# Optimization experiments

Hardware: AMD Instinct MI355X
Metric: run time of the kernel (lower is better)

Reference implementation:

```python
import jax, jax.numpy as jnp
import numpy as np

P_X, P_H, P_L, P_VT, P_ET, B = 512, 1024, 4, 512, 256, 512
IN_DIM = P_X + 2 * P_H  # concat([x, prev_time_h, prev_layer_h])


def setup_inputs() -> dict:
    key = jax.random.key(0)
    ks = jax.random.split(key, 10)
    sc_in = 1.0 / np.sqrt(IN_DIM)
    sc_lh = 1.0 / np.sqrt(P_L * P_H)
    return {
        "input_x": jax.random.normal(ks[0], (B, P_X), jnp.float32),
        "h_prev": jax.random.normal(ks[1], (P_L, B, P_H), jnp.float32),
        "c_prev": jax.random.normal(ks[2], (P_L, B, P_H), jnp.float32),
        # stacked gate weights: [L, 4 gates (i,f,o,s), h, in_dim]
        "Wg": jax.random.uniform(ks[3], (P_L, 4, P_H, IN_DIM), jnp.float32, -sc_in, sc_in),
        "bg": jax.random.uniform(ks[4], (P_L, 4, P_H), jnp.float32, -sc_in, sc_in),
        "W_y": jax.random.uniform(ks[5], (P_VT, P_L * P_H), jnp.float32, -sc_lh, sc_lh),
        "b_y": jax.random.uniform(ks[6], (P_VT,), jnp.float32, -sc_lh, sc_lh),
        "W_E": jax.random.uniform(ks[7], (P_ET, P_L * P_H), jnp.float32, -sc_lh, sc_lh),
        "b_E": jax.random.uniform(ks[8], (P_ET,), jnp.float32, -sc_lh, sc_lh),
    }


def _controller(input_x, h_prev, c_prev, Wg, bg):
    prev_layer = jnp.zeros((input_x.shape[0], P_H), input_x.dtype)
    hiddens = []
    for i in range(P_L):  # loop over small fixed layer count
        z = jnp.concatenate([input_x, h_prev[i], prev_layer], axis=-1)  # [B, IN_DIM]
        g = jnp.einsum("bd,ghd->bgh", z, Wg[i]) + bg[i]  # [B, 4, H], one fused GEMM
        i_g = jax.nn.sigmoid(g[:, 0])
        f_g = jax.nn.sigmoid(g[:, 1])
        o_g = jax.nn.sigmoid(g[:, 2])
        s_g = jnp.tanh(g[:, 3])
        c_new = f_g * c_prev[i] + i_g * s_g
        h_new = o_g * jnp.tanh(c_new)
        hiddens.append(h_new)
        prev_layer = h_new
    return jnp.concatenate(hiddens, axis=-1)  # [B, L*H]


def reference(input_x, h_prev, c_prev, Wg, bg, W_y, b_y, W_E, b_E):
    hidden = _controller(input_x, h_prev, c_prev, Wg, bg)
    output = hidden @ W_y.T + b_y      # [B, v_t]
    interface = hidden @ W_E.T + b_E   # [B, E_t]
    return (output, interface)
```

## Files before the change

kernel.cpp:

```cpp
#include <hip/hip_runtime.h>


typedef short    shortx8  __attribute__((ext_vector_type(8)));
typedef float    floatx4  __attribute__((ext_vector_type(4)));
typedef float    floatx16 __attribute__((ext_vector_type(16)));

__device__ __forceinline__ unsigned int f2bf1(float x) {
  unsigned int u = __float_as_uint(x);
  return (u + 0x7fffu + ((u >> 16) & 1u)) >> 16;
}
__device__ __forceinline__ unsigned int f2bf2(float lo, float hi) {
  return f2bf1(lo) | (f2bf1(hi) << 16);
}
__device__ __forceinline__ float sigm(float x) { return 1.f / (1.f + __expf(-x)); }
__device__ __forceinline__ float tanh_(float x) { return 1.f - 2.f / (__expf(2.f * x) + 1.f); }

__global__ __launch_bounds__(256) void prep_a0(const float* __restrict__ x,
                                               const float* __restrict__ hp,
                                               unsigned short* __restrict__ A0) {
  const int l   = blockIdx.y;
  const int idx = blockIdx.x * 256 + threadIdx.x;
  const int b   = idx / 192;
  const int kk  = (idx - b * 192) * 8;
  float v[8];
  if (kk < 512) {
    const float* s = x + (size_t)b * 512 + kk;
#pragma unroll
    for (int i = 0; i < 8; ++i) v[i] = s[i];
  } else {
    const float* s = hp + ((size_t)l * 512 + b) * 1024 + (kk - 512);
#pragma unroll
    for (int i = 0; i < 8; ++i) v[i] = s[i];
  }
  uint4 o;
  o.x = f2bf2(v[0], v[1]); o.y = f2bf2(v[2], v[3]);
  o.z = f2bf2(v[4], v[5]); o.w = f2bf2(v[6], v[7]);
  *(uint4*)(A0 + ((size_t)l * 512 + b) * 1536 + kk) = o;
}

__global__ __launch_bounds__(256) void conv_wseq(const float* __restrict__ Wg,
                                                 unsigned short* __restrict__ Wseq) {
  const int idx = blockIdx.x * 256 + threadIdx.x;
  const int row = idx >> 7;
  const int k0  = (idx & 127) * 8;
  const int l   = (row >> 12) + 1;
  const int n   = row & 4095;
  const float* s = Wg + (size_t)l * 4096 * 2560 + (size_t)n * 2560 + 1536 + k0;
  const float4 v0 = *(const float4*)(s);
  const float4 v1 = *(const float4*)(s + 4);
  uint4 o;
  o.x = f2bf2(v0.x, v0.y); o.y = f2bf2(v0.z, v0.w);
  o.z = f2bf2(v1.x, v1.y); o.w = f2bf2(v1.z, v1.w);
  *(uint4*)(Wseq + (size_t)row * 1024 + k0) = o;
}

__global__ __launch_bounds__(256, 2) void gemm_gates(
    const unsigned short* __restrict__ A0, const float* __restrict__ Wg,
    const float* __restrict__ bg, float* __restrict__ G) {
  __shared__ __align__(16) unsigned short As[2][128 * 64];
  __shared__ __align__(16) unsigned short Bs[2][128 * 64];
  const int tid = threadIdx.x, lane = tid & 63, wave = tid >> 6;
  const int raw   = blockIdx.x + 4 * (blockIdx.y + 32 * blockIdx.z);
  const int xcd   = raw & 7, slot = raw >> 3;
  const int nl    = (slot >> 2) * 8 + xcd;
  const int mbase = (slot & 3) * 128;
  const int nbase = (nl & 31) * 128;
  const int l     = nl >> 5;
  const unsigned short* Ab = A0 + ((size_t)l * 512 + mbase) * 1536;
  const float*          Bb = Wg + (size_t)l * 4096 * 2560 + (size_t)nbase * 2560;
  const int arow = wave * 8 + (lane >> 3);
  const int akg  = lane & 7;

  uint4  apf[4];
  float4 bpf[8];
  auto loadT = [&](int kt) {
    const int kg = kt * 64;
#pragma unroll
    for (int r = 0; r < 4; ++r)
      apf[r] = *(const uint4*)(Ab + (size_t)(arow + r * 32) * 1536 + kg + akg * 8);
#pragma unroll
    for (int j = 0; j < 8; ++j) {
      const int idx = j * 256 + tid;
      bpf[j] = *(const float4*)(Bb + (size_t)(idx >> 4) * 2560 + kg + (idx & 15) * 4);
    }
  };
  auto storeT = [&](int buf) {
#pragma unroll
    for (int r = 0; r < 4; ++r) {
      const int row = arow + r * 32;
      *(uint4*)(&As[buf][row * 64 + ((akg ^ (row & 7)) * 8)]) = apf[r];
    }
#pragma unroll
    for (int j = 0; j < 8; ++j) {
      const int idx = j * 256 + tid;
      const int n = idx >> 4, kc = (idx & 15) * 4;
      uint2 pk;
      pk.x = f2bf2(bpf[j].x, bpf[j].y);
      pk.y = f2bf2(bpf[j].z, bpf[j].w);
      *(uint2*)(&Bs[buf][n * 64 + (((kc >> 3) ^ (n & 7)) * 8) + (kc & 4)]) = pk;
    }
  };

  floatx16 acc[2][2];
#pragma unroll
  for (int a = 0; a < 2; ++a)
#pragma unroll
    for (int b2 = 0; b2 < 2; ++b2)
#pragma unroll
      for (int r = 0; r < 16; ++r) acc[a][b2][r] = 0.f;

  const int wm = (wave >> 1) * 64, wn = (wave & 1) * 64;
  loadT(0);
  storeT(0);
  __syncthreads();
  for (int kt = 0; kt < 24; ++kt) {
    if (kt + 1 < 24) loadT(kt + 1);
    const int cb = kt & 1;
#pragma unroll
    for (int ks = 0; ks < 4; ++ks) {
      const int gb = ks * 2 + (lane >> 5);
      shortx8 af[2], bfv[2];
#pragma unroll
      for (int sm = 0; sm < 2; ++sm) {
        const int row = wm + sm * 32 + (lane & 31);
        af[sm] = *(const shortx8*)(&As[cb][row * 64 + ((gb ^ (row & 7)) * 8)]);
      }
#pragma unroll
      for (int sn = 0; sn < 2; ++sn) {
        const int row = wn + sn * 32 + (lane & 31);
        bfv[sn] = *(const shortx8*)(&Bs[cb][row * 64 + ((gb ^ (row & 7)) * 8)]);
      }
#pragma unroll
      for (int sm = 0; sm < 2; ++sm)
#pragma unroll
        for (int sn = 0; sn < 2; ++sn)
          acc[sm][sn] = __builtin_amdgcn_mfma_f32_32x32x16_bf16(
              af[sm], bfv[sn], acc[sm][sn], 0, 0, 0);
    }
    if (kt + 1 < 24) storeT((kt + 1) & 1);
    __syncthreads();
  }

  const float* bgl = bg + (size_t)l * 4096;
  float* Gl = G + ((size_t)l * 512 + mbase) * 4096;
#pragma unroll
  for (int sm = 0; sm < 2; ++sm)
#pragma unroll
    for (int sn = 0; sn < 2; ++sn) {
      const int col = nbase + wn + sn * 32 + (lane & 31);
      const float bias = bgl[col];
#pragma unroll
      for (int r = 0; r < 16; ++r) {
        const int row = wm + sm * 32 + ((r & 3) + 8 * (r >> 2) + 4 * (lane >> 5));
        Gl[(size_t)row * 4096 + col] = acc[sm][sn][r] + bias;
      }
    }
}

__global__ __launch_bounds__(256) void cell0(const float* __restrict__ G,
                                             const float* __restrict__ cp_l,
                                             unsigned short* __restrict__ hidden) {
  const int idx = (blockIdx.x * 256 + threadIdx.x) * 4;
  const int b = idx >> 10, h = idx & 1023;
  const float* g0 = G + (size_t)b * 4096;
  const float4 vi = *(const float4*)(g0 + h);
  const float4 vf = *(const float4*)(g0 + 1024 + h);
  const float4 vo = *(const float4*)(g0 + 2048 + h);
  const float4 vs = *(const float4*)(g0 + 3072 + h);
  const float4 cp = *(const float4*)(cp_l + (size_t)b * 1024 + h);
  const float gi[4] = {vi.x, vi.y, vi.z, vi.w};
  const float gf[4] = {vf.x, vf.y, vf.z, vf.w};
  const float go[4] = {vo.x, vo.y, vo.z, vo.w};
  const float gs[4] = {vs.x, vs.y, vs.z, vs.w};
  const float cc[4] = {cp.x, cp.y, cp.z, cp.w};
  float hn[4];
#pragma unroll
  for (int j = 0; j < 4; ++j) {
    const float c = sigm(gf[j]) * cc[j] + sigm(gi[j]) * tanh_(gs[j]);
    hn[j] = sigm(go[j]) * tanh_(c);
  }
  uint2 o;
  o.x = f2bf2(hn[0], hn[1]);
  o.y = f2bf2(hn[2], hn[3]);
  *(uint2*)(hidden + (size_t)b * 4096 + h) = o;
}

__global__ __launch_bounds__(256) void seq_stream(
    const unsigned short* __restrict__ hidden_ro,
    const unsigned short* __restrict__ Wseq,
    const float* __restrict__ G, const float* __restrict__ c_prev,
    unsigned short* __restrict__ hidden_w, int l) {
  const int tid = threadIdx.x, lane = tid & 63, wv = tid >> 6;
  const int bid = blockIdx.x;
  const int x   = bid & 7;
  const int mg  = (bid >> 3) & 7;
  const int t   = bid >> 6;
  const int ht  = x * 8 + t;
  const int mt  = mg * 4 + wv;
  const int mb  = mt * 16, h0 = ht * 16;
  const int lrow = lane & 15, lg = lane >> 4;

  const unsigned short* Ab = hidden_ro + (size_t)(mb + lrow) * 4096
                             + (size_t)(l - 1) * 1024 + lg * 8;
  const unsigned short* Bb = Wseq + (size_t)(l - 1) * 4194304
                             + (size_t)(h0 + lrow) * 1024 + lg * 8;

  const int brow = mb + lg * 4;
  const int hg   = h0 + lrow;
  float gvv[4][4];
  float cold[4];
#pragma unroll
  for (int r = 0; r < 4; ++r) {
    const float* Gb = G + ((size_t)l * 512 + brow + r) * 4096 + hg;
#pragma unroll
    for (int g = 0; g < 4; ++g) gvv[g][r] = Gb[g * 1024];
    cold[r] = c_prev[((size_t)l * 512 + brow + r) * 1024 + hg];
  }

  floatx4 acc0, acc1, acc2, acc3;
#pragma unroll
  for (int r = 0; r < 4; ++r) { acc0[r] = 0.f; acc1[r] = 0.f; acc2[r] = 0.f; acc3[r] = 0.f; }

  shortx8 a0, a1, a2, a3;
  shortx8 b00, b01, b02, b03;
  shortx8 b10, b11, b12, b13;
  shortx8 b20, b21, b22, b23;
  shortx8 b30, b31, b32, b33;

#define LD_SET(ai, b0_, b1_, b2_, b3_, kt)                                   \
  {                                                                          \
    const int ko = (kt) * 32;                                                \
    ai  = *(const shortx8*)(Ab + ko);                                        \
    b0_ = *(const shortx8*)(Bb + ko);                                        \
    b1_ = *(const shortx8*)(Bb + 1048576 + ko);                              \
    b2_ = *(const shortx8*)(Bb + 2097152 + ko);                              \
    b3_ = *(const shortx8*)(Bb + 3145728 + ko);                              \
  }
#define C_SET(ai, b0_, b1_, b2_, b3_)                                        \
  {                                                                          \
    acc0 = __builtin_amdgcn_mfma_f32_16x16x32_bf16(ai, b0_, acc0, 0, 0, 0);  \
    acc1 = __builtin_amdgcn_mfma_f32_16x16x32_bf16(ai, b1_, acc1, 0, 0, 0);  \
    acc2 = __builtin_amdgcn_mfma_f32_16x16x32_bf16(ai, b2_, acc2, 0, 0, 0);  \
    acc3 = __builtin_amdgcn_mfma_f32_16x16x32_bf16(ai, b3_, acc3, 0, 0, 0);  \
  }

  LD_SET(a0, b00, b01, b02, b03, 0)
  LD_SET(a1, b10, b11, b12, b13, 1)
  LD_SET(a2, b20, b21, b22, b23, 2)
  LD_SET(a3, b30, b31, b32, b33, 3)
#pragma unroll 1
  for (int kt4 = 0; kt4 < 8; ++kt4) {
    const int kt = kt4 * 4;
    C_SET(a0, b00, b01, b02, b03)
    if (kt + 4 < 32) LD_SET(a0, b00, b01, b02, b03, kt + 4)
    C_SET(a1, b10, b11, b12, b13)
    if (kt + 5 < 32) LD_SET(a1, b10, b11, b12, b13, kt + 5)
    C_SET(a2, b20, b21, b22, b23)
    if (kt + 6 < 32) LD_SET(a2, b20, b21, b22, b23, kt + 6)
    C_SET(a3, b30, b31, b32, b33)
    if (kt + 7 < 32) LD_SET(a3, b30, b31, b32, b33, kt + 7)
  }
#undef LD_SET
#undef C_SET

#pragma unroll
  for (int r = 0; r < 4; ++r) {
    const float gi = acc0[r] + gvv[0][r];
    const float gf = acc1[r] + gvv[1][r];
    const float go = acc2[r] + gvv[2][r];
    const float gs = acc3[r] + gvv[3][r];
    const float c  = sigm(gf) * cold[r] + sigm(gi) * tanh_(gs);
    const float hn = sigm(go) * tanh_(c);
    hidden_w[(size_t)(brow + r) * 4096 + l * 1024 + hg] = (unsigned short)f2bf1(hn);
  }
}

__global__ __launch_bounds__(256) void gemm_heads(
    const unsigned short* __restrict__ A, const float* __restrict__ Wy,
    const float* __restrict__ WE, float* __restrict__ Cp) {
  __shared__ __align__(16) unsigned short As[2][128 * 64];
  __shared__ __align__(16) unsigned short Bs[2][128 * 64];
  const int tid = threadIdx.x, lane = tid & 63, wave = tid >> 6;
  const int rawb = blockIdx.x + 8 * (blockIdx.y + 6 * blockIdx.z);
  const int xcd  = rawb & 7, slot = rawb >> 3;
  const int pair = (slot >> 2) * 8 + xcd;
  const int mbase  = (slot & 3) * 128;
  const int ksplit = pair & 7;
  const int nt     = pair >> 3;
  const int nbase  = nt * 128;
  const float* Bb = (nt < 4) ? (Wy + (size_t)nbase * 4096)
                             : (WE + (size_t)(nbase - 512) * 4096);
  const int k0 = ksplit * 512;
  const unsigned short* Ab = A + (size_t)mbase * 4096;
  const int arow = wave * 8 + (lane >> 3);
  const int akg  = lane & 7;

  uint4  apf[4];
  float4 bpf[8];
  auto loadT = [&](int kt) {
    const int kg = k0 + kt * 64;
#pragma unroll
    for (int r = 0; r < 4; ++r)
      apf[r] = *(const uint4*)(Ab + (size_t)(arow + r * 32) * 4096 + kg + akg * 8);
#pragma unroll
    for (int j = 0; j < 8; ++j) {
      const int idx = j * 256 + tid;
      bpf[j] = *(const float4*)(Bb + (size_t)(idx >> 4) * 4096 + kg + (idx & 15) * 4);
    }
  };
  auto storeT = [&](int buf) {
#pragma unroll
    for (int r = 0; r < 4; ++r) {
      const int row = arow + r * 32;
      *(uint4*)(&As[buf][row * 64 + ((akg ^ (row & 7)) * 8)]) = apf[r];
    }
#pragma unroll
    for (int j = 0; j < 8; ++j) {
      const int idx = j * 256 + tid;
      const int n = idx >> 4, kc = (idx & 15) * 4;
      uint2 pk;
      pk.x = f2bf2(bpf[j].x, bpf[j].y);
      pk.y = f2bf2(bpf[j].z, bpf[j].w);
      *(uint2*)(&Bs[buf][n * 64 + (((kc >> 3) ^ (n & 7)) * 8) + (kc & 4)]) = pk;
    }
  };

  floatx16 acc[2][2];
#pragma unroll
  for (int a = 0; a < 2; ++a)
#pragma unroll
    for (int b2 = 0; b2 < 2; ++b2)
#pragma unroll
      for (int r = 0; r < 16; ++r) acc[a][b2][r] = 0.f;
  const int wm = (wave >> 1) * 64, wn = (wave & 1) * 64;

  loadT(0);
  storeT(0);
  __syncthreads();
  for (int kt = 0; kt < 8; ++kt) {
    if (kt + 1 < 8) loadT(kt + 1);
    const int cb = kt & 1;
#pragma unroll
    for (int ks = 0; ks < 4; ++ks) {
      const int gb = ks * 2 + (lane >> 5);
      shortx8 af[2], bfv[2];
#pragma unroll
      for (int sm = 0; sm < 2; ++sm) {
        const int row = wm + sm * 32 + (lane & 31);
        af[sm] = *(const shortx8*)(&As[cb][row * 64 + ((gb ^ (row & 7)) * 8)]);
      }
#pragma unroll
      for (int sn = 0; sn < 2; ++sn) {
        const int row = wn + sn * 32 + (lane & 31);
        bfv[sn] = *(const shortx8*)(&Bs[cb][row * 64 + ((gb ^ (row & 7)) * 8)]);
      }
#pragma unroll
      for (int sm = 0; sm < 2; ++sm)
#pragma unroll
        for (int sn = 0; sn < 2; ++sn)
          acc[sm][sn] = __builtin_amdgcn_mfma_f32_32x32x16_bf16(
              af[sm], bfv[sn], acc[sm][sn], 0, 0, 0);
    }
    if (kt + 1 < 8) storeT((kt + 1) & 1);
    __syncthreads();
  }

  float* Co = Cp + (size_t)ksplit * 512 * 768;
#pragma unroll
  for (int sm = 0; sm < 2; ++sm)
#pragma unroll
    for (int sn = 0; sn < 2; ++sn) {
      const int col = nbase + wn + sn * 32 + (lane & 31);
#pragma unroll
      for (int r = 0; r < 16; ++r) {
        const int row = mbase + wm + sm * 32 +
                        ((r & 3) + 8 * (r >> 2) + 4 * (lane >> 5));
        Co[(size_t)row * 768 + col] = acc[sm][sn][r];
      }
    }
}

__global__ __launch_bounds__(256) void head_reduce(
    const float* __restrict__ hp, const float* __restrict__ b_y,
    const float* __restrict__ b_E, float* __restrict__ out) {
  const int n = blockIdx.x * 256 + threadIdx.x;
  const int b = blockIdx.y;
  float s = 0.f;
#pragma unroll
  for (int ks = 0; ks < 8; ++ks)
    s += hp[(size_t)ks * 512 * 768 + (size_t)b * 768 + n];
  if (n < 512)
    out[(size_t)b * 512 + n] = s + b_y[n];
  else
    out[(size_t)512 * 512 + (size_t)b * 256 + (n - 512)] = s + b_E[n - 512];
}

extern "C" void kernel_launch(void* const* d_in, const int* in_sizes, int n_in,
                              void* d_out, int out_size, void* d_ws, size_t ws_size,
                              hipStream_t stream) {
  const float* x      = (const float*)d_in[0];
  const float* h_prev = (const float*)d_in[1];
  const float* c_prev = (const float*)d_in[2];
  const float* Wg     = (const float*)d_in[3];
  const float* bg     = (const float*)d_in[4];
  const float* W_y    = (const float*)d_in[5];
  const float* b_y    = (const float*)d_in[6];
  const float* W_E    = (const float*)d_in[7];
  const float* b_E    = (const float*)d_in[8];

  char* ws = (char*)d_ws;
  unsigned short* A0     = (unsigned short*)(ws + 0);
  float*          G      = (float*)(ws + 6291456);
  unsigned short* hidden = (unsigned short*)(ws + 39845888);
  unsigned short* Wseq   = (unsigned short*)(ws + 44040192);
  float*          hpart  = (float*)(ws + 44040192);

  conv_wseq<<<dim3(6144), 256, 0, stream>>>(Wg, Wseq);
  prep_a0<<<dim3(384, 4), 256, 0, stream>>>(x, h_prev, A0);
  gemm_gates<<<dim3(4, 32, 4), 256, 0, stream>>>(A0, Wg, bg, G);
  cell0<<<512, 256, 0, stream>>>(G, c_prev, hidden);
  for (int l = 1; l < 4; ++l)
    seq_stream<<<dim3(512), 256, 0, stream>>>(hidden, Wseq, G, c_prev,
                                              hidden, l);
  gemm_heads<<<dim3(8, 6, 4), 256, 0, stream>>>(hidden, W_y, W_E, hpart);
  head_reduce<<<dim3(3, 512), 256, 0, stream>>>(hpart, b_y, b_E, (float*)d_out);
}
```

Before: 460.3 us.

## Pre-convert all weights to bf16 and stage GEMM tiles via global_load_lds

A single prep kernel now converts all of Wg, W_y and W_E to bf16, together with the A0 activations, replacing the separate conv_wseq and prep_a0 launches. The gates and heads GEMMs then read bf16 weights and stage tiles straight into LDS with global_load_lds, which drops the register round-trip and the in-loop fp32-to-bf16 conversion. seq_stream reads its recurrent weights from the fully converted Wg buffer. In exchange, the prep pass reads and writes far more data, including the unused prev-layer slice of layer 0, and the LDS XOR swizzle is gone, so fragment reads may hit bank conflicts.

Measured after the change: 478.2 us. +3.9%, slower.

```diff
diff --git a/kernel.cpp b/kernel.cpp
--- a/kernel.cpp
+++ b/kernel.cpp
@@ -5,6 +5,11 @@
 typedef float    floatx4  __attribute__((ext_vector_type(4)));
 typedef float    floatx16 __attribute__((ext_vector_type(16)));
 
+#define GLOAD16(SRC, DST)                                                    \
+  __builtin_amdgcn_global_load_lds(                                          \
+      (const __attribute__((address_space(1))) unsigned int*)(SRC),          \
+      (__attribute__((address_space(3))) unsigned int*)(DST), 16, 0, 0)
+
 __device__ __forceinline__ unsigned int f2bf1(float x) {
   unsigned int u = __float_as_uint(x);
   return (u + 0x7fffu + ((u >> 16) & 1u)) >> 16;
@@ -15,47 +20,51 @@
 __device__ __forceinline__ float sigm(float x) { return 1.f / (1.f + __expf(-x)); }
 __device__ __forceinline__ float tanh_(float x) { return 1.f - 2.f / (__expf(2.f * x) + 1.f); }
 
-__global__ __launch_bounds__(256) void prep_a0(const float* __restrict__ x,
-                                               const float* __restrict__ hp,
-                                               unsigned short* __restrict__ A0) {
-  const int l   = blockIdx.y;
-  const int idx = blockIdx.x * 256 + threadIdx.x;
-  const int b   = idx / 192;
-  const int kk  = (idx - b * 192) * 8;
-  float v[8];
-  if (kk < 512) {
-    const float* s = x + (size_t)b * 512 + kk;
-#pragma unroll
-    for (int i = 0; i < 8; ++i) v[i] = s[i];
+__global__ __launch_bounds__(256) void prep_all(
+    const float* __restrict__ x, const float* __restrict__ hp,
+    const float* __restrict__ Wg, const float* __restrict__ Wy,
+    const float* __restrict__ WE, unsigned short* __restrict__ A0,
+    unsigned short* __restrict__ Wc, unsigned short* __restrict__ Wyc,
+    unsigned short* __restrict__ WEc) {
+  const int bid = blockIdx.x;
+  if (bid < 22016) {
+    const size_t i8 = ((size_t)bid * 256 + threadIdx.x) * 8;
+    const float* s;
+    unsigned short* d;
+    if (i8 < 41943040u) { s = Wg + i8; d = Wc + i8; }
+    else if (i8 < 44040192u) { s = Wy + (i8 - 41943040u); d = Wyc + (i8 - 41943040u); }
+    else { s = WE + (i8 - 44040192u); d = WEc + (i8 - 44040192u); }
+    const float4 v0 = *(const float4*)(s);
+    const float4 v1 = *(const float4*)(s + 4);
+    uint4 o;
+    o.x = f2bf2(v0.x, v0.y); o.y = f2bf2(v0.z, v0.w);
+    o.z = f2bf2(v1.x, v1.y); o.w = f2bf2(v1.z, v1.w);
+    *(uint4*)(d) = o;
   } else {
-    const float* s = hp + ((size_t)l * 512 + b) * 1024 + (kk - 512);
-#pragma unroll
-    for (int i = 0; i < 8; ++i) v[i] = s[i];
-  }
-  uint4 o;
-  o.x = f2bf2(v[0], v[1]); o.y = f2bf2(v[2], v[3]);
-  o.z = f2bf2(v[4], v[5]); o.w = f2bf2(v[6], v[7]);
-  *(uint4*)(A0 + ((size_t)l * 512 + b) * 1536 + kk) = o;
-}
-
-__global__ __launch_bounds__(256) void conv_wseq(const float* __restrict__ Wg,
-                                                 unsigned short* __restrict__ Wseq) {
-  const int idx = blockIdx.x * 256 + threadIdx.x;
-  const int row = idx >> 7;
-  const int k0  = (idx & 127) * 8;
-  const int l   = (row >> 12) + 1;
-  const int n   = row & 4095;
-  const float* s = Wg + (size_t)l * 4096 * 2560 + (size_t)n * 2560 + 1536 + k0;
-  const float4 v0 = *(const float4*)(s);
-  const float4 v1 = *(const float4*)(s + 4);
-  uint4 o;
-  o.x = f2bf2(v0.x, v0.y); o.y = f2bf2(v0.z, v0.w);
-  o.z = f2bf2(v1.x, v1.y); o.w = f2bf2(v1.z, v1.w);
-  *(uint4*)(Wseq + (size_t)row * 1024 + k0) = o;
+    const int j   = (bid - 22016) * 256 + threadIdx.x;
+    const int l   = j / 98304;
+    const int rem = j - l * 98304;
+    const int b   = rem / 192;
+    const int kk  = (rem - b * 192) * 8;
+    float v[8];
+    if (kk < 512) {
+      const float* s = x + (size_t)b * 512 + kk;
+#pragma unroll
+      for (int i = 0; i < 8; ++i) v[i] = s[i];
+    } else {
+      const float* s = hp + ((size_t)l * 512 + b) * 1024 + (kk - 512);
+#pragma unroll
+      for (int i = 0; i < 8; ++i) v[i] = s[i];
+    }
+    uint4 o;
+    o.x = f2bf2(v[0], v[1]); o.y = f2bf2(v[2], v[3]);
+    o.z = f2bf2(v[4], v[5]); o.w = f2bf2(v[6], v[7]);
+    *(uint4*)(A0 + ((size_t)l * 512 + b) * 1536 + kk) = o;
+  }
 }
 
 __global__ __launch_bounds__(256, 2) void gemm_gates(
-    const unsigned short* __restrict__ A0, const float* __restrict__ Wg,
+    const unsigned short* __restrict__ A0, const unsigned short* __restrict__ Wc,
     const float* __restrict__ bg, float* __restrict__ G) {
   __shared__ __align__(16) unsigned short As[2][128 * 64];
   __shared__ __align__(16) unsigned short Bs[2][128 * 64];
@@ -67,39 +76,22 @@
   const int nbase = (nl & 31) * 128;
   const int l     = nl >> 5;
   const unsigned short* Ab = A0 + ((size_t)l * 512 + mbase) * 1536;
-  const float*          Bb = Wg + (size_t)l * 4096 * 2560 + (size_t)nbase * 2560;
-  const int arow = wave * 8 + (lane >> 3);
-  const int akg  = lane & 7;
-
-  uint4  apf[4];
-  float4 bpf[8];
-  auto loadT = [&](int kt) {
+  const unsigned short* Bb = Wc + (size_t)l * 4096 * 2560 + (size_t)nbase * 2560;
+  const int wv8 = wave * 8;
+  const int lr  = lane >> 3;
+  const int lc  = (lane & 7) * 8;
+
+  auto stage = [&](int kt, int buf) {
     const int kg = kt * 64;
 #pragma unroll
     for (int r = 0; r < 4; ++r)
-      apf[r] = *(const uint4*)(Ab + (size_t)(arow + r * 32) * 1536 + kg + akg * 8);
-#pragma unroll
-    for (int j = 0; j < 8; ++j) {
-      const int idx = j * 256 + tid;
-      bpf[j] = *(const float4*)(Bb + (size_t)(idx >> 4) * 2560 + kg + (idx & 15) * 4);
-    }
+      GLOAD16(Ab + (size_t)(wv8 + lr + r * 32) * 1536 + kg + lc,
+              &As[buf][(wv8 + r * 32) * 64]);
+#pragma unroll
+    for (int r = 0; r < 4; ++r)
+      GLOAD16(Bb + (size_t)(wv8 + lr + r * 32) * 2560 + kg + lc,
+              &Bs[buf][(wv8 + r * 32) * 64]);
   };
-  auto storeT = [&](int buf) {
-#pragma unroll
-    for (int r = 0; r < 4; ++r) {
-      const int row = arow + r * 32;
-      *(uint4*)(&As[buf][row * 64 + ((akg ^ (row & 7)) * 8)]) = apf[r];
-    }
-#pragma unroll
-    for (int j = 0; j < 8; ++j) {
-      const int idx = j * 256 + tid;
-      const int n = idx >> 4, kc = (idx & 15) * 4;
-      uint2 pk;
-      pk.x = f2bf2(bpf[j].x, bpf[j].y);
-      pk.y = f2bf2(bpf[j].z, bpf[j].w);
-      *(uint2*)(&Bs[buf][n * 64 + (((kc >> 3) ^ (n & 7)) * 8) + (kc & 4)]) = pk;
-    }
-  };
 
   floatx16 acc[2][2];
 #pragma unroll
@@ -110,26 +102,17 @@
       for (int r = 0; r < 16; ++r) acc[a][b2][r] = 0.f;
 
   const int wm = (wave >> 1) * 64, wn = (wave & 1) * 64;
-  loadT(0);
-  storeT(0);
-  __syncthreads();
-  for (int kt = 0; kt < 24; ++kt) {
-    if (kt + 1 < 24) loadT(kt + 1);
-    const int cb = kt & 1;
+  auto compute = [&](int cb) {
 #pragma unroll
     for (int ks = 0; ks < 4; ++ks) {
       const int gb = ks * 2 + (lane >> 5);
       shortx8 af[2], bfv[2];
 #pragma unroll
-      for (int sm = 0; sm < 2; ++sm) {
-        const int row = wm + sm * 32 + (lane & 31);
-        af[sm] = *(const shortx8*)(&As[cb][row * 64 + ((gb ^ (row & 7)) * 8)]);
-      }
-#pragma unroll
-      for (int sn = 0; sn < 2; ++sn) {
-        const int row = wn + sn * 32 + (lane & 31);
-        bfv[sn] = *(const shortx8*)(&Bs[cb][row * 64 + ((gb ^ (row & 7)) * 8)]);
-      }
+      for (int sm = 0; sm < 2; ++sm)
+        af[sm] = *(const shortx8*)(&As[cb][(wm + sm * 32 + (lane & 31)) * 64 + gb * 8]);
+#pragma unroll
+      for (int sn = 0; sn < 2; ++sn)
+        bfv[sn] = *(const shortx8*)(&Bs[cb][(wn + sn * 32 + (lane & 31)) * 64 + gb * 8]);
 #pragma unroll
       for (int sm = 0; sm < 2; ++sm)
 #pragma unroll
@@ -137,7 +120,14 @@
           acc[sm][sn] = __builtin_amdgcn_mfma_f32_32x32x16_bf16(
               af[sm], bfv[sn], acc[sm][sn], 0, 0, 0);
     }
-    if (kt + 1 < 24) storeT((kt + 1) & 1);
+  };
+
+  stage(0, 0);
+  __syncthreads();
+#pragma unroll 1
+  for (int kt = 0; kt < 24; ++kt) {
+    if (kt + 1 < 24) stage(kt + 1, (kt + 1) & 1);
+    compute(kt & 1);
     __syncthreads();
   }
 
@@ -187,7 +177,7 @@
 
 __global__ __launch_bounds__(256) void seq_stream(
     const unsigned short* __restrict__ hidden_ro,
-    const unsigned short* __restrict__ Wseq,
+    const unsigned short* __restrict__ Wc,
     const float* __restrict__ G, const float* __restrict__ c_prev,
     unsigned short* __restrict__ hidden_w, int l) {
   const int tid = threadIdx.x, lane = tid & 63, wv = tid >> 6;
@@ -202,8 +192,8 @@
 
   const unsigned short* Ab = hidden_ro + (size_t)(mb + lrow) * 4096
                              + (size_t)(l - 1) * 1024 + lg * 8;
-  const unsigned short* Bb = Wseq + (size_t)(l - 1) * 4194304
-                             + (size_t)(h0 + lrow) * 1024 + lg * 8;
+  const unsigned short* Bb = Wc + (size_t)l * 4096 * 2560
+                             + (size_t)(h0 + lrow) * 2560 + 1536 + lg * 8;
 
   const int brow = mb + lg * 4;
   const int hg   = h0 + lrow;
@@ -232,9 +222,9 @@
     const int ko = (kt) * 32;                                                \
     ai  = *(const shortx8*)(Ab + ko);                                        \
     b0_ = *(const shortx8*)(Bb + ko);                                        \
-    b1_ = *(const shortx8*)(Bb + 1048576 + ko);                              \
-    b2_ = *(const shortx8*)(Bb + 2097152 + ko);                              \
-    b3_ = *(const shortx8*)(Bb + 3145728 + ko);                              \
+    b1_ = *(const shortx8*)(Bb + 2621440 + ko);                              \
+    b2_ = *(const shortx8*)(Bb + 5242880 + ko);                              \
+    b3_ = *(const shortx8*)(Bb + 7864320 + ko);                              \
   }
 #define C_SET(ai, b0_, b1_, b2_, b3_)                                        \
   {                                                                          \
@@ -275,9 +265,9 @@
   }
 }
 
-__global__ __launch_bounds__(256) void gemm_heads(
-    const unsigned short* __restrict__ A, const float* __restrict__ Wy,
-    const float* __restrict__ WE, float* __restrict__ Cp) {
+__global__ __launch_bounds__(256, 2) void gemm_heads(
+    const unsigned short* __restrict__ A, const unsigned short* __restrict__ Wyc,
+    const unsigned short* __restrict__ WEc, float* __restrict__ Cp) {
   __shared__ __align__(16) unsigned short As[2][128 * 64];
   __shared__ __align__(16) unsigned short Bs[2][128 * 64];
   const int tid = threadIdx.x, lane = tid & 63, wave = tid >> 6;
@@ -288,41 +278,24 @@
   const int ksplit = pair & 7;
   const int nt     = pair >> 3;
   const int nbase  = nt * 128;
-  const float* Bb = (nt < 4) ? (Wy + (size_t)nbase * 4096)
-                             : (WE + (size_t)(nbase - 512) * 4096);
+  const unsigned short* Bb = (nt < 4) ? (Wyc + (size_t)nbase * 4096)
+                                      : (WEc + (size_t)(nbase - 512) * 4096);
   const int k0 = ksplit * 512;
   const unsigned short* Ab = A + (size_t)mbase * 4096;
-  const int arow = wave * 8 + (lane >> 3);
-  const int akg  = lane & 7;
-
-  uint4  apf[4];
-  float4 bpf[8];
-  auto loadT = [&](int kt) {
+  const int wv8 = wave * 8;
+  const int lr  = lane >> 3;
+  const int lc  = (lane & 7) * 8;
+
+  auto stage = [&](int kt, int buf) {
     const int kg = k0 + kt * 64;
 #pragma unroll
     for (int r = 0; r < 4; ++r)
-      apf[r] = *(const uint4*)(Ab + (size_t)(arow + r * 32) * 4096 + kg + akg * 8);
-#pragma unroll
-    for (int j = 0; j < 8; ++j) {
-      const int idx = j * 256 + tid;
-      bpf[j] = *(const float4*)(Bb + (size_t)(idx >> 4) * 4096 + kg + (idx & 15) * 4);
-    }
-  };
-  auto storeT = [&](int buf) {
-#pragma unroll
-    for (int r = 0; r < 4; ++r) {
-      const int row = arow + r * 32;
-      *(uint4*)(&As[buf][row * 64 + ((akg ^ (row & 7)) * 8)]) = apf[r];
-    }
-#pragma unroll
-    for (int j = 0; j < 8; ++j) {
-      const int idx = j * 256 + tid;
-      const int n = idx >> 4, kc = (idx & 15) * 4;
-      uint2 pk;
-      pk.x = f2bf2(bpf[j].x, bpf[j].y);
-      pk.y = f2bf2(bpf[j].z, bpf[j].w);
-      *(uint2*)(&Bs[buf][n * 64 + (((kc >> 3) ^ (n & 7)) * 8) + (kc & 4)]) = pk;
-    }
+      GLOAD16(Ab + (size_t)(wv8 + lr + r * 32) * 4096 + kg + lc,
+              &As[buf][(wv8 + r * 32) * 64]);
+#pragma unroll
+    for (int r = 0; r < 4; ++r)
+      GLOAD16(Bb + (size_t)(wv8 + lr + r * 32) * 4096 + kg + lc,
+              &Bs[buf][(wv8 + r * 32) * 64]);
   };
 
   floatx16 acc[2][2];
@@ -334,26 +307,17 @@
       for (int r = 0; r < 16; ++r) acc[a][b2][r] = 0.f;
   const int wm = (wave >> 1) * 64, wn = (wave & 1) * 64;
 
-  loadT(0);
-  storeT(0);
-  __syncthreads();
-  for (int kt = 0; kt < 8; ++kt) {
-    if (kt + 1 < 8) loadT(kt + 1);
-    const int cb = kt & 1;
+  auto compute = [&](int cb) {
 #pragma unroll
     for (int ks = 0; ks < 4; ++ks) {
       const int gb = ks * 2 + (lane >> 5);
       shortx8 af[2], bfv[2];
 #pragma unroll
-      for (int sm = 0; sm < 2; ++sm) {
-        const int row = wm + sm * 32 + (lane & 31);
-        af[sm] = *(const shortx8*)(&As[cb][row * 64 + ((gb ^ (row & 7)) * 8)]);
-      }
-#pragma unroll
-      for (int sn = 0; sn < 2; ++sn) {
-        const int row = wn + sn * 32 + (lane & 31);
-        bfv[sn] = *(const shortx8*)(&Bs[cb][row * 64 + ((gb ^ (row & 7)) * 8)]);
-      }
+      for (int sm = 0; sm < 2; ++sm)
+        af[sm] = *(const shortx8*)(&As[cb][(wm + sm * 32 + (lane & 31)) * 64 + gb * 8]);
+#pragma unroll
+      for (int sn = 0; sn < 2; ++sn)
+        bfv[sn] = *(const shortx8*)(&Bs[cb][(wn + sn * 32 + (lane & 31)) * 64 + gb * 8]);
 #pragma unroll
       for (int sm = 0; sm < 2; ++sm)
 #pragma unroll
@@ -361,7 +325,14 @@
           acc[sm][sn] = __builtin_amdgcn_mfma_f32_32x32x16_bf16(
               af[sm], bfv[sn], acc[sm][sn], 0, 0, 0);
     }
-    if (kt + 1 < 8) storeT((kt + 1) & 1);
+  };
+
+  stage(0, 0);
+  __syncthreads();
+#pragma unroll 1
+  for (int kt = 0; kt < 8; ++kt) {
+    if (kt + 1 < 8) stage(kt + 1, (kt + 1) & 1);
+    compute(kt & 1);
     __syncthreads();
   }
 
@@ -412,16 +383,18 @@
   unsigned short* A0     = (unsigned short*)(ws + 0);
   float*          G      = (float*)(ws + 6291456);
   unsigned short* hidden = (unsigned short*)(ws + 39845888);
-  unsigned short* Wseq   = (unsigned short*)(ws + 44040192);
+  unsigned short* Wc     = (unsigned short*)(ws + 44040192);
   float*          hpart  = (float*)(ws + 44040192);
-
-  conv_wseq<<<dim3(6144), 256, 0, stream>>>(Wg, Wseq);
-  prep_a0<<<dim3(384, 4), 256, 0, stream>>>(x, h_prev, A0);
-  gemm_gates<<<dim3(4, 32, 4), 256, 0, stream>>>(A0, Wg, bg, G);
+  unsigned short* Wyc    = (unsigned short*)(ws + 127926272);
+  unsigned short* WEc    = (unsigned short*)(ws + 132120576);
+
+  prep_all<<<dim3(23552), 256, 0, stream>>>(x, h_prev, Wg, W_y, W_E,
+                                            A0, Wc, Wyc, WEc);
+  gemm_gates<<<dim3(4, 32, 4), 256, 0, stream>>>(A0, Wc, bg, G);
   cell0<<<512, 256, 0, stream>>>(G, c_prev, hidden);
   for (int l = 1; l < 4; ++l)
-    seq_stream<<<dim3(512), 256, 0, stream>>>(hidden, Wseq, G, c_prev,
+    seq_stream<<<dim3(512), 256, 0, stream>>>(hidden, Wc, G, c_prev,
                                               hidden, l);
-  gemm_heads<<<dim3(8, 6, 4), 256, 0, stream>>>(hidden, W_y, W_E, hpart);
+  gemm_heads<<<dim3(8, 6, 4), 256, 0, stream>>>(hidden, Wyc, WEc, hpart);
   head_reduce<<<dim3(3, 512), 256, 0, stream>>>(hpart, b_y, b_E, (float*)d_out);
 }
```
